# Kernel tuning notes

Measured on AMD Instinct MI355X. Metric: run time of the kernel, lower is better.

## Reference

```python
import jax, jax.numpy as jnp
import numpy as np

GRID_SHAPE = (32, 32)
TEMPERATURE = 1.0


def setup_inputs() -> dict:
    key = jax.random.key(0)
    k1, k2 = jax.random.split(key)
    x = jax.random.normal(k1, (16384, 1024), dtype=jnp.float32)
    som_weights = jax.random.normal(k2, (*GRID_SHAPE, 1024), dtype=jnp.float32) * 0.05
    return {"x": x, "som_weights": som_weights}


def reference(x, som_weights):
    # x: [B, D]; som_weights: [G1, G2, D]
    B, D = x.shape
    g1, g2 = GRID_SHAPE
    w_flat = som_weights.reshape(g1 * g2, D)  # [N, D]
    x_sq = jnp.sum(x * x, axis=-1, keepdims=True)          # [B, 1]
    w_sq = jnp.sum(w_flat * w_flat, axis=-1)[None, :]       # [1, N]
    d2 = x_sq - 2.0 * (x @ w_flat.T) + w_sq                 # [B, N]
    logits = (-d2 / TEMPERATURE).reshape(B, g1, g2)         # [B, G1, G2]
    # per-dimension softmax along each spatial axis, combined multiplicatively
    s1 = jax.nn.softmax(logits, axis=1)
    s2 = jax.nn.softmax(logits, axis=2)
    combined = s1 * s2
    combined = combined / (jnp.sum(combined, axis=(1, 2), keepdims=True) + 1e-8)
    # soft reconstruction: weighted sum over grid of codebook vectors
    recon = jnp.einsum('bn,nd->bd', combined.reshape(B, g1 * g2), w_flat)
    return recon
```

## Files before the change

kernel.cpp:

```cpp
#include <hip/hip_runtime.h>
#include <hip/hip_bf16.h>

static constexpr int BATCH = 16384;
static constexpr int DIM   = 1024;
static constexpr int NN    = 1024;

typedef _Float16 half8  __attribute__((ext_vector_type(8)));
typedef _Float16 half4v __attribute__((ext_vector_type(4)));
typedef float    f32x4  __attribute__((ext_vector_type(4)));

static constexpr float L2E = 1.44269504088896340736f;

__global__ __launch_bounds__(256) void cvt_x_kernel(const float* __restrict__ x,
                                                    _Float16* __restrict__ xh) {
    size_t i = ((size_t)blockIdx.x * 256 + threadIdx.x) * 8;
    f32x4 a = *(const f32x4*)(x + i);
    f32x4 b = *(const f32x4*)(x + i + 4);
    half8 h;
#pragma unroll
    for (int q = 0; q < 4; ++q) { h[q] = (_Float16)a[q]; h[4 + q] = (_Float16)b[q]; }
    *(half8*)(xh + i) = h;
}

__global__ __launch_bounds__(256) void prep_pack_kernel(const float* __restrict__ W,
                                                        _Float16* __restrict__ P1,
                                                        _Float16* __restrict__ P2) {
    const int l = threadIdx.x & 63;
    const int v = threadIdx.x >> 6;
    const int f = blockIdx.x * 4 + v;
    const int hi = f >> 5, lo = f & 31;
    {
        int n  = hi * 16 + (l & 15);
        int k0 = lo * 32 + (l >> 4) * 8;
        const float* src = W + (size_t)n * DIM + k0;
        f32x4 a = *(const f32x4*)src;
        f32x4 b = *(const f32x4*)(src + 4);
        half8 h;
#pragma unroll
        for (int q = 0; q < 4; ++q) { h[q] = (_Float16)a[q]; h[4 + q] = (_Float16)b[q]; }
        *(half8*)(P1 + ((size_t)f * 64 + l) * 8) = h;
    }
    {
        int d  = hi * 16 + (l & 15);
        int n0 = lo * 32 + (l >> 4) * 8;
        half8 h;
#pragma unroll
        for (int j = 0; j < 8; ++j) h[j] = (_Float16)W[(size_t)(n0 + j) * DIM + d];
        *(half8*)(P2 + ((size_t)f * 64 + l) * 8) = h;
    }
}

__global__ __launch_bounds__(256) void wsq_kernel(const float* __restrict__ W,
                                                  float* __restrict__ wsq) {
    const int n = blockIdx.x;
    const int t = threadIdx.x;
    float4 v = *(const float4*)(W + (size_t)n * DIM + 4 * t);
    float ss = v.x * v.x + v.y * v.y + v.z * v.z + v.w * v.w;
#pragma unroll
    for (int o = 32; o > 0; o >>= 1) ss += __shfl_xor(ss, o, 64);
    __shared__ float red[4];
    if ((t & 63) == 0) red[t >> 6] = ss;
    __syncthreads();
    if (t == 0) wsq[n] = red[0] + red[1] + red[2] + red[3];
}

__global__ __launch_bounds__(512, 2) void fused_som_kernel(
    const _Float16* __restrict__ Xh, const _Float16* __restrict__ P1,
    const _Float16* __restrict__ P2, const float* __restrict__ wsq,
    float* __restrict__ Out) {

    __shared__ __align__(16) _Float16 xs[2][64 * 64];
    __shared__ __align__(16) char     BIG[131072];
    __shared__ __align__(16) float    a1_lds[64 * 32];

    const int t  = threadIdx.x;
    const int l  = t & 63;
    const int w  = t >> 6;
    const int r0 = blockIdx.x * 64;

    auto stageA = [&](int buf, int kt) {
        int row = t >> 3;
        int c   = (t & 7) ^ (row & 7);
        const _Float16* g = Xh + (size_t)(r0 + row) * DIM + kt + c * 8;
        __builtin_amdgcn_global_load_lds(
            (const __attribute__((address_space(1))) void*)g,
            (__attribute__((address_space(3))) void*)(&xs[buf][(w * 8) * 64]),
            16, 0, 0);
    };

    f32x4 acc[4][8] = {};
    stageA(0, 0);
    __syncthreads();

    for (int kt = 0; kt < DIM; kt += 64) {
        const int cur = (kt >> 6) & 1;
        const int tk0 = kt >> 5;
        half8 bf0[8], bf1[8];
#pragma unroll
        for (int ni = 0; ni < 8; ++ni) {
            const size_t fb = (size_t)(w * 8 + ni) * 32;
            bf0[ni] = *(const half8*)(P1 + ((fb + tk0) * 64 + l) * 8);
            bf1[ni] = *(const half8*)(P1 + ((fb + tk0 + 1) * 64 + l) * 8);
        }
        if (kt + 64 < DIM) stageA(cur ^ 1, kt + 64);
        half8 af[4];
#pragma unroll
        for (int mi = 0; mi < 4; ++mi) {
            const _Float16* pa = &xs[cur][((l & 15) + mi * 16) * 64];
            af[mi] = *(const half8*)(pa + ((0 + (l >> 4)) ^ (l & 7)) * 8);
        }
#pragma unroll
        for (int mi = 0; mi < 4; ++mi)
#pragma unroll
            for (int ni = 0; ni < 8; ++ni)
                acc[mi][ni] = __builtin_amdgcn_mfma_f32_16x16x32_f16(
                    af[mi], bf0[ni], acc[mi][ni], 0, 0, 0);
#pragma unroll
        for (int mi = 0; mi < 4; ++mi) {
            const _Float16* pa = &xs[cur][((l & 15) + mi * 16) * 64];
            af[mi] = *(const half8*)(pa + ((4 + (l >> 4)) ^ (l & 7)) * 8);
        }
#pragma unroll
        for (int mi = 0; mi < 4; ++mi)
#pragma unroll
            for (int ni = 0; ni < 8; ++ni)
                acc[mi][ni] = __builtin_amdgcn_mfma_f32_16x16x32_f16(
                    af[mi], bf1[ni], acc[mi][ni], 0, 0, 0);
        __syncthreads();
    }

    float wq[8];
#pragma unroll
    for (int ni = 0; ni < 8; ++ni) wq[ni] = wsq[w * 128 + ni * 16 + (l & 15)];
#pragma unroll
    for (int mi = 0; mi < 4; ++mi)
#pragma unroll
        for (int ni = 0; ni < 8; ++ni)
#pragma unroll
            for (int q = 0; q < 4; ++q)
                acc[mi][ni][q] = 2.f * acc[mi][ni][q] - wq[ni];

    float* red = (float*)BIG;

    f32x4 a2v[4][4];
#pragma unroll
    for (int mi = 0; mi < 4; ++mi)
#pragma unroll
        for (int p = 0; p < 4; ++p) {
            f32x4 mx;
#pragma unroll
            for (int q = 0; q < 4; ++q)
                mx[q] = fmaxf(acc[mi][2 * p][q], acc[mi][2 * p + 1][q]);
#pragma unroll
            for (int q = 0; q < 4; ++q) {
                float m = mx[q];
                m = fmaxf(m, __shfl_xor(m, 1, 64));
                m = fmaxf(m, __shfl_xor(m, 2, 64));
                m = fmaxf(m, __shfl_xor(m, 4, 64));
                m = fmaxf(m, __shfl_xor(m, 8, 64));
                mx[q] = m;
            }
#pragma unroll
            for (int q = 0; q < 4; ++q) {
                float s = exp2f((acc[mi][2 * p][q] - mx[q]) * L2E) +
                          exp2f((acc[mi][2 * p + 1][q] - mx[q]) * L2E);
                s += __shfl_xor(s, 1, 64);
                s += __shfl_xor(s, 2, 64);
                s += __shfl_xor(s, 4, 64);
                s += __shfl_xor(s, 8, 64);
                a2v[mi][p][q] = mx[q] * L2E + log2f(s);
            }
        }

#pragma unroll
    for (int mi = 0; mi < 4; ++mi)
#pragma unroll
        for (int j = 0; j < 2; ++j)
#pragma unroll
            for (int q = 0; q < 4; ++q) {
                float pm = fmaxf(fmaxf(acc[mi][j][q], acc[mi][2 + j][q]),
                                 fmaxf(acc[mi][4 + j][q], acc[mi][6 + j][q]));
                int row = mi * 16 + (l >> 4) * 4 + q;
                red[(w * 64 + row) * 33 + j * 16 + (l & 15)] = pm;
            }
    __syncthreads();
#pragma unroll
    for (int i = 0; i < 4; ++i) {
        int pr = t + i * 512;
        int row = pr >> 5, g2 = pr & 31;
        float m = red[row * 33 + g2];
#pragma unroll
        for (int wv = 1; wv < 8; ++wv)
            m = fmaxf(m, red[(wv * 64 + row) * 33 + g2]);
        a1_lds[row * 32 + g2] = m;
    }
    __syncthreads();
#pragma unroll
    for (int mi = 0; mi < 4; ++mi)
#pragma unroll
        for (int j = 0; j < 2; ++j)
#pragma unroll
            for (int q = 0; q < 4; ++q) {
                int row = mi * 16 + (l >> 4) * 4 + q;
                float m1 = a1_lds[row * 32 + j * 16 + (l & 15)];
                float s = 0.f;
#pragma unroll
                for (int p = 0; p < 4; ++p)
                    s += exp2f((acc[mi][2 * p + j][q] - m1) * L2E);
                red[(w * 64 + row) * 33 + j * 16 + (l & 15)] = s;
            }
    __syncthreads();
#pragma unroll
    for (int i = 0; i < 4; ++i) {
        int pr = t + i * 512;
        int row = pr >> 5, g2 = pr & 31;
        float s = 0.f;
#pragma unroll
        for (int wv = 0; wv < 8; ++wv)
            s += red[(wv * 64 + row) * 33 + g2];
        a1_lds[row * 32 + g2] = a1_lds[row * 32 + g2] * L2E + log2f(s);
    }
    __syncthreads();

    float* rowred = (float*)BIG;
#pragma unroll
    for (int mi = 0; mi < 4; ++mi) {
        f32x4 rs = {0.f, 0.f, 0.f, 0.f};
#pragma unroll
        for (int j = 0; j < 2; ++j) {
            f32x4 a1v;
#pragma unroll
            for (int q = 0; q < 4; ++q) {
                int row = mi * 16 + (l >> 4) * 4 + q;
                a1v[q] = a1_lds[row * 32 + j * 16 + (l & 15)];
            }
#pragma unroll
            for (int p = 0; p < 4; ++p)
#pragma unroll
                for (int q = 0; q < 4; ++q) {
                    float cu = exp2f(acc[mi][2 * p + j][q] * (2.f * L2E)
                                     - a1v[q] - a2v[mi][p][q]);
                    acc[mi][2 * p + j][q] = cu;
                    rs[q] += cu;
                }
        }
#pragma unroll
        for (int q = 0; q < 4; ++q) {
            float sv = rs[q];
            sv += __shfl_xor(sv, 1, 64);
            sv += __shfl_xor(sv, 2, 64);
            sv += __shfl_xor(sv, 4, 64);
            sv += __shfl_xor(sv, 8, 64);
            if ((l & 15) == 0) rowred[w * 64 + mi * 16 + (l >> 4) * 4 + q] = sv;
        }
    }
    __syncthreads();
    float* rowinv = ((float*)BIG) + 512;
    if (t < 64) {
        float tot = 0.f;
#pragma unroll
        for (int wv = 0; wv < 8; ++wv) tot += rowred[wv * 64 + t];
        rowinv[t] = 1.f / (tot + 1e-8f);
    }
    __syncthreads();
    f32x4 invr[4];
#pragma unroll
    for (int mi = 0; mi < 4; ++mi)
#pragma unroll
        for (int q = 0; q < 4; ++q)
            invr[mi][q] = rowinv[mi * 16 + (l >> 4) * 4 + q];
    __syncthreads();

    _Float16* cs = (_Float16*)BIG;
#pragma unroll
    for (int mi = 0; mi < 4; ++mi)
#pragma unroll
        for (int ni = 0; ni < 8; ++ni) {
            int chunk = w * 16 + ni * 2 + ((l & 15) >> 3);
#pragma unroll
            for (int q = 0; q < 4; ++q) {
                int row = mi * 16 + (l >> 4) * 4 + q;
                cs[row * 1024 + (chunk ^ (row & 7)) * 8 + (l & 7)] =
                    (_Float16)(acc[mi][ni][q] * invr[mi][q]);
            }
        }
    __syncthreads();

    f32x4 acc2[4][8] = {};
#pragma unroll 2
    for (int kt = 0; kt < NN; kt += 32) {
        const int tn = kt >> 5;
        half8 bf[8], af2[4];
#pragma unroll
        for (int ni = 0; ni < 8; ++ni)
            bf[ni] = *(const half8*)(P2 +
                (((size_t)(w * 8 + ni) * 32 + tn) * 64 + l) * 8);
#pragma unroll
        for (int mi = 0; mi < 4; ++mi) {
            int row = (l & 15) + mi * 16;
            int kc  = tn * 4 + (l >> 4);
            af2[mi] = *(const half8*)(cs + row * 1024 + (kc ^ (row & 7)) * 8);
        }
#pragma unroll
        for (int mi = 0; mi < 4; ++mi)
#pragma unroll
            for (int ni = 0; ni < 8; ++ni)
                acc2[mi][ni] = __builtin_amdgcn_mfma_f32_16x16x32_f16(
                    af2[mi], bf[ni], acc2[mi][ni], 0, 0, 0);
    }

#pragma unroll
    for (int mi = 0; mi < 4; ++mi) {
        const int rbase = r0 + mi * 16 + (l >> 4) * 4;
#pragma unroll
        for (int ni = 0; ni < 8; ++ni) {
            const int col = w * 128 + ni * 16 + (l & 15);
#pragma unroll
            for (int q = 0; q < 4; ++q)
                Out[(size_t)(rbase + q) * DIM + col] = acc2[mi][ni][q];
        }
    }
}

extern "C" void kernel_launch(void* const* d_in, const int* in_sizes, int n_in,
                              void* d_out, int out_size, void* d_ws, size_t ws_size,
                              hipStream_t stream) {
    const float* x = (const float*)d_in[0];
    const float* w = (const float*)d_in[1];
    float* out = (float*)d_out;

    char* ws = (char*)d_ws;
    size_t off = 0;
    _Float16* xh    = (_Float16*)(ws + off); off += (size_t)BATCH * DIM * 2;
    _Float16* pack1 = (_Float16*)(ws + off); off += (size_t)NN * DIM * 2;
    _Float16* pack2 = (_Float16*)(ws + off); off += (size_t)DIM * NN * 2;
    float*    wsq   = (float*)   (ws + off); off += (size_t)NN * 4;

    cvt_x_kernel<<<(BATCH * DIM) / (256 * 8), 256, 0, stream>>>(x, xh);
    prep_pack_kernel<<<512, 256, 0, stream>>>(w, pack1, pack2);
    wsq_kernel<<<NN, 256, 0, stream>>>(w, wsq);
    fused_som_kernel<<<BATCH / 64, 512, 0, stream>>>(xh, pack1, pack2, wsq, out);
}
```

Baseline: 227.4 us.

## Fuse x conversion into main kernel and widen blocks to 1024 threads

Removes the separate fp32-to-fp16 conversion kernel for x. The main kernel now loads fp32 x directly with nontemporal loads, converts it in registers and writes it into the swizzled LDS buffer. It doubles the block size to 16 waves, each covering 64 columns instead of 128, which halves per-thread accumulators. It also writes unnormalized softmax products straight into LDS and applies the row normalization at output time, with nontemporal stores. The aim is to save the extra round trip of the x conversion and one LDS pass, at the risk of more LDS pressure and heavier cross-wave reduction work per block.

```diff
diff --git a/kernel.cpp b/kernel.cpp
--- a/kernel.cpp
+++ b/kernel.cpp
@@ -1,5 +1,4 @@
 #include <hip/hip_runtime.h>
-#include <hip/hip_bf16.h>
 
 static constexpr int BATCH = 16384;
 static constexpr int DIM   = 1024;
@@ -10,17 +9,6 @@
 typedef float    f32x4  __attribute__((ext_vector_type(4)));
 
 static constexpr float L2E = 1.44269504088896340736f;
-
-__global__ __launch_bounds__(256) void cvt_x_kernel(const float* __restrict__ x,
-                                                    _Float16* __restrict__ xh) {
-    size_t i = ((size_t)blockIdx.x * 256 + threadIdx.x) * 8;
-    f32x4 a = *(const f32x4*)(x + i);
-    f32x4 b = *(const f32x4*)(x + i + 4);
-    half8 h;
-#pragma unroll
-    for (int q = 0; q < 4; ++q) { h[q] = (_Float16)a[q]; h[4 + q] = (_Float16)b[q]; }
-    *(half8*)(xh + i) = h;
-}
 
 __global__ __launch_bounds__(256) void prep_pack_kernel(const float* __restrict__ W,
                                                         _Float16* __restrict__ P1,
@@ -64,55 +52,75 @@
     if (t == 0) wsq[n] = red[0] + red[1] + red[2] + red[3];
 }
 
-__global__ __launch_bounds__(512, 2) void fused_som_kernel(
-    const _Float16* __restrict__ Xh, const _Float16* __restrict__ P1,
+__global__ __launch_bounds__(1024, 4) void fused_som_kernel(
+    const float* __restrict__ X, const _Float16* __restrict__ P1,
     const _Float16* __restrict__ P2, const float* __restrict__ wsq,
     float* __restrict__ Out) {
 
     __shared__ __align__(16) _Float16 xs[2][64 * 64];
     __shared__ __align__(16) char     BIG[131072];
     __shared__ __align__(16) float    a1_lds[64 * 32];
+    __shared__ __align__(16) float    rowred[16 * 64];
+    __shared__ __align__(16) float    rowinv[64];
 
     const int t  = threadIdx.x;
     const int l  = t & 63;
     const int w  = t >> 6;
     const int r0 = blockIdx.x * 64;
 
-    auto stageA = [&](int buf, int kt) {
-        int row = t >> 3;
-        int c   = (t & 7) ^ (row & 7);
-        const _Float16* g = Xh + (size_t)(r0 + row) * DIM + kt + c * 8;
-        __builtin_amdgcn_global_load_lds(
-            (const __attribute__((address_space(1))) void*)g,
-            (__attribute__((address_space(3))) void*)(&xs[buf][(w * 8) * 64]),
-            16, 0, 0);
+    auto RIDX = [](int wv, int row, int g2) {
+        return (wv * 64 + row) * 32 + (g2 ^ ((row & 4) << 2));
     };
-
-    f32x4 acc[4][8] = {};
-    stageA(0, 0);
+    auto AIDX = [](int row, int g2) {
+        return row * 32 + (g2 ^ ((row & 4) << 2));
+    };
+
+    const int srow = t >> 4;
+    const int skq  = t & 15;
+
+    auto xload = [&](int kt) -> f32x4 {
+        return __builtin_nontemporal_load(
+            (const f32x4*)(X + (size_t)(r0 + srow) * DIM + kt + skq * 4));
+    };
+    auto xwrite = [&](int buf, f32x4 v) {
+        half4v h;
+        h[0] = (_Float16)v[0]; h[1] = (_Float16)v[1];
+        h[2] = (_Float16)v[2]; h[3] = (_Float16)v[3];
+        int c = skq >> 1;
+        *(half4v*)&xs[buf][srow * 64 + ((c ^ (srow & 7)) << 3) + ((skq & 1) << 2)] = h;
+    };
+
+    f32x4 acc[4][4] = {};
+    {
+        f32x4 xv = xload(0);
+        xwrite(0, xv);
+    }
     __syncthreads();
 
     for (int kt = 0; kt < DIM; kt += 64) {
         const int cur = (kt >> 6) & 1;
+        const bool hasNext = (kt + 64 < DIM);
+        f32x4 xv;
+        if (hasNext) xv = xload(kt + 64);
+
         const int tk0 = kt >> 5;
-        half8 bf0[8], bf1[8];
-#pragma unroll
-        for (int ni = 0; ni < 8; ++ni) {
-            const size_t fb = (size_t)(w * 8 + ni) * 32;
+        half8 bf0[4], bf1[4];
+#pragma unroll
+        for (int ni = 0; ni < 4; ++ni) {
+            const size_t fb = (size_t)(w * 4 + ni) * 32;
             bf0[ni] = *(const half8*)(P1 + ((fb + tk0) * 64 + l) * 8);
             bf1[ni] = *(const half8*)(P1 + ((fb + tk0 + 1) * 64 + l) * 8);
         }
-        if (kt + 64 < DIM) stageA(cur ^ 1, kt + 64);
         half8 af[4];
 #pragma unroll
         for (int mi = 0; mi < 4; ++mi) {
             const _Float16* pa = &xs[cur][((l & 15) + mi * 16) * 64];
-            af[mi] = *(const half8*)(pa + ((0 + (l >> 4)) ^ (l & 7)) * 8);
+            af[mi] = *(const half8*)(pa + (((l >> 4)) ^ (l & 7)) * 8);
         }
 #pragma unroll
         for (int mi = 0; mi < 4; ++mi)
 #pragma unroll
-            for (int ni = 0; ni < 8; ++ni)
+            for (int ni = 0; ni < 4; ++ni)
                 acc[mi][ni] = __builtin_amdgcn_mfma_f32_16x16x32_f16(
                     af[mi], bf0[ni], acc[mi][ni], 0, 0, 0);
 #pragma unroll
@@ -123,30 +131,32 @@
 #pragma unroll
         for (int mi = 0; mi < 4; ++mi)
 #pragma unroll
-            for (int ni = 0; ni < 8; ++ni)
+            for (int ni = 0; ni < 4; ++ni)
                 acc[mi][ni] = __builtin_amdgcn_mfma_f32_16x16x32_f16(
                     af[mi], bf1[ni], acc[mi][ni], 0, 0, 0);
+        __builtin_amdgcn_sched_barrier(0);
+        if (hasNext) xwrite(cur ^ 1, xv);
         __syncthreads();
     }
 
-    float wq[8];
-#pragma unroll
-    for (int ni = 0; ni < 8; ++ni) wq[ni] = wsq[w * 128 + ni * 16 + (l & 15)];
+    float wq[4];
+#pragma unroll
+    for (int ni = 0; ni < 4; ++ni) wq[ni] = wsq[w * 64 + ni * 16 + (l & 15)];
 #pragma unroll
     for (int mi = 0; mi < 4; ++mi)
 #pragma unroll
-        for (int ni = 0; ni < 8; ++ni)
+        for (int ni = 0; ni < 4; ++ni)
 #pragma unroll
             for (int q = 0; q < 4; ++q)
                 acc[mi][ni][q] = 2.f * acc[mi][ni][q] - wq[ni];
 
     float* red = (float*)BIG;
 
-    f32x4 a2v[4][4];
+    f32x4 a2v[4][2];
 #pragma unroll
     for (int mi = 0; mi < 4; ++mi)
 #pragma unroll
-        for (int p = 0; p < 4; ++p) {
+        for (int p = 0; p < 2; ++p) {
             f32x4 mx;
 #pragma unroll
             for (int q = 0; q < 4; ++q)
@@ -178,21 +188,19 @@
         for (int j = 0; j < 2; ++j)
 #pragma unroll
             for (int q = 0; q < 4; ++q) {
-                float pm = fmaxf(fmaxf(acc[mi][j][q], acc[mi][2 + j][q]),
-                                 fmaxf(acc[mi][4 + j][q], acc[mi][6 + j][q]));
                 int row = mi * 16 + (l >> 4) * 4 + q;
-                red[(w * 64 + row) * 33 + j * 16 + (l & 15)] = pm;
-            }
-    __syncthreads();
-#pragma unroll
-    for (int i = 0; i < 4; ++i) {
-        int pr = t + i * 512;
+                red[RIDX(w, row, j * 16 + (l & 15))] =
+                    fmaxf(acc[mi][j][q], acc[mi][2 + j][q]);
+            }
+    __syncthreads();
+#pragma unroll
+    for (int i = 0; i < 2; ++i) {
+        int pr = t + i * 1024;
         int row = pr >> 5, g2 = pr & 31;
-        float m = red[row * 33 + g2];
-#pragma unroll
-        for (int wv = 1; wv < 8; ++wv)
-            m = fmaxf(m, red[(wv * 64 + row) * 33 + g2]);
-        a1_lds[row * 32 + g2] = m;
+        float m = red[RIDX(0, row, g2)];
+#pragma unroll
+        for (int wv = 1; wv < 16; ++wv) m = fmaxf(m, red[RIDX(wv, row, g2)]);
+        a1_lds[AIDX(row, g2)] = m;
     }
     __syncthreads();
 #pragma unroll
@@ -202,27 +210,24 @@
 #pragma unroll
             for (int q = 0; q < 4; ++q) {
                 int row = mi * 16 + (l >> 4) * 4 + q;
-                float m1 = a1_lds[row * 32 + j * 16 + (l & 15)];
-                float s = 0.f;
-#pragma unroll
-                for (int p = 0; p < 4; ++p)
-                    s += exp2f((acc[mi][2 * p + j][q] - m1) * L2E);
-                red[(w * 64 + row) * 33 + j * 16 + (l & 15)] = s;
-            }
-    __syncthreads();
-#pragma unroll
-    for (int i = 0; i < 4; ++i) {
-        int pr = t + i * 512;
+                float m1 = a1_lds[AIDX(row, j * 16 + (l & 15))];
+                float s = exp2f((acc[mi][j][q] - m1) * L2E) +
+                          exp2f((acc[mi][2 + j][q] - m1) * L2E);
+                red[RIDX(w, row, j * 16 + (l & 15))] = s;
+            }
+    __syncthreads();
+#pragma unroll
+    for (int i = 0; i < 2; ++i) {
+        int pr = t + i * 1024;
         int row = pr >> 5, g2 = pr & 31;
         float s = 0.f;
 #pragma unroll
-        for (int wv = 0; wv < 8; ++wv)
-            s += red[(wv * 64 + row) * 33 + g2];
-        a1_lds[row * 32 + g2] = a1_lds[row * 32 + g2] * L2E + log2f(s);
-    }
-    __syncthreads();
-
-    float* rowred = (float*)BIG;
+        for (int wv = 0; wv < 16; ++wv) s += red[RIDX(wv, row, g2)];
+        a1_lds[AIDX(row, g2)] = a1_lds[AIDX(row, g2)] * L2E + log2f(s);
+    }
+    __syncthreads();
+
+    _Float16* cs = (_Float16*)BIG;
 #pragma unroll
     for (int mi = 0; mi < 4; ++mi) {
         f32x4 rs = {0.f, 0.f, 0.f, 0.f};
@@ -232,17 +237,23 @@
 #pragma unroll
             for (int q = 0; q < 4; ++q) {
                 int row = mi * 16 + (l >> 4) * 4 + q;
-                a1v[q] = a1_lds[row * 32 + j * 16 + (l & 15)];
-            }
-#pragma unroll
-            for (int p = 0; p < 4; ++p)
+                a1v[q] = a1_lds[AIDX(row, j * 16 + (l & 15))];
+            }
+#pragma unroll
+            for (int p = 0; p < 2; ++p) {
+                int ni  = 2 * p + j;
+                int col = w * 64 + ni * 16 + (l & 15);
+                int chunk = col >> 3;
 #pragma unroll
                 for (int q = 0; q < 4; ++q) {
-                    float cu = exp2f(acc[mi][2 * p + j][q] * (2.f * L2E)
+                    float cu = exp2f(acc[mi][ni][q] * (2.f * L2E)
                                      - a1v[q] - a2v[mi][p][q]);
-                    acc[mi][2 * p + j][q] = cu;
                     rs[q] += cu;
+                    int row = mi * 16 + (l >> 4) * 4 + q;
+                    cs[row * 1024 + ((chunk ^ (row & 7)) << 3) + (col & 7)] =
+                        (_Float16)cu;
                 }
+            }
         }
 #pragma unroll
         for (int q = 0; q < 4; ++q) {
@@ -255,69 +266,51 @@
         }
     }
     __syncthreads();
-    float* rowinv = ((float*)BIG) + 512;
+
     if (t < 64) {
         float tot = 0.f;
 #pragma unroll
-        for (int wv = 0; wv < 8; ++wv) tot += rowred[wv * 64 + t];
+        for (int wv = 0; wv < 16; ++wv) tot += rowred[wv * 64 + t];
         rowinv[t] = 1.f / (tot + 1e-8f);
     }
-    __syncthreads();
-    f32x4 invr[4];
-#pragma unroll
-    for (int mi = 0; mi < 4; ++mi)
-#pragma unroll
-        for (int q = 0; q < 4; ++q)
-            invr[mi][q] = rowinv[mi * 16 + (l >> 4) * 4 + q];
-    __syncthreads();
-
-    _Float16* cs = (_Float16*)BIG;
-#pragma unroll
-    for (int mi = 0; mi < 4; ++mi)
-#pragma unroll
-        for (int ni = 0; ni < 8; ++ni) {
-            int chunk = w * 16 + ni * 2 + ((l & 15) >> 3);
-#pragma unroll
-            for (int q = 0; q < 4; ++q) {
-                int row = mi * 16 + (l >> 4) * 4 + q;
-                cs[row * 1024 + (chunk ^ (row & 7)) * 8 + (l & 7)] =
-                    (_Float16)(acc[mi][ni][q] * invr[mi][q]);
-            }
-        }
-    __syncthreads();
-
-    f32x4 acc2[4][8] = {};
+
+    f32x4 acc2[4][4] = {};
 #pragma unroll 2
     for (int kt = 0; kt < NN; kt += 32) {
         const int tn = kt >> 5;
-        half8 bf[8], af2[4];
-#pragma unroll
-        for (int ni = 0; ni < 8; ++ni)
+        half8 bf[4], af2[4];
+#pragma unroll
+        for (int ni = 0; ni < 4; ++ni)
             bf[ni] = *(const half8*)(P2 +
-                (((size_t)(w * 8 + ni) * 32 + tn) * 64 + l) * 8);
+                (((size_t)(w * 4 + ni) * 32 + tn) * 64 + l) * 8);
 #pragma unroll
         for (int mi = 0; mi < 4; ++mi) {
             int row = (l & 15) + mi * 16;
             int kc  = tn * 4 + (l >> 4);
-            af2[mi] = *(const half8*)(cs + row * 1024 + (kc ^ (row & 7)) * 8);
+            af2[mi] = *(const half8*)(cs + row * 1024 + ((kc ^ (row & 7)) << 3));
         }
 #pragma unroll
         for (int mi = 0; mi < 4; ++mi)
 #pragma unroll
-            for (int ni = 0; ni < 8; ++ni)
+            for (int ni = 0; ni < 4; ++ni)
                 acc2[mi][ni] = __builtin_amdgcn_mfma_f32_16x16x32_f16(
                     af2[mi], bf[ni], acc2[mi][ni], 0, 0, 0);
     }
+    __syncthreads();
 
 #pragma unroll
     for (int mi = 0; mi < 4; ++mi) {
         const int rbase = r0 + mi * 16 + (l >> 4) * 4;
-#pragma unroll
-        for (int ni = 0; ni < 8; ++ni) {
-            const int col = w * 128 + ni * 16 + (l & 15);
+        f32x4 inv;
+#pragma unroll
+        for (int q = 0; q < 4; ++q) inv[q] = rowinv[mi * 16 + (l >> 4) * 4 + q];
+#pragma unroll
+        for (int ni = 0; ni < 4; ++ni) {
+            const int col = w * 64 + ni * 16 + (l & 15);
 #pragma unroll
             for (int q = 0; q < 4; ++q)
-                Out[(size_t)(rbase + q) * DIM + col] = acc2[mi][ni][q];
+                __builtin_nontemporal_store(acc2[mi][ni][q] * inv[q],
+                    Out + (size_t)(rbase + q) * DIM + col);
         }
     }
 }
@@ -331,13 +324,11 @@
 
     char* ws = (char*)d_ws;
     size_t off = 0;
-    _Float16* xh    = (_Float16*)(ws + off); off += (size_t)BATCH * DIM * 2;
     _Float16* pack1 = (_Float16*)(ws + off); off += (size_t)NN * DIM * 2;
     _Float16* pack2 = (_Float16*)(ws + off); off += (size_t)DIM * NN * 2;
     float*    wsq   = (float*)   (ws + off); off += (size_t)NN * 4;
 
-    cvt_x_kernel<<<(BATCH * DIM) / (256 * 8), 256, 0, stream>>>(x, xh);
     prep_pack_kernel<<<512, 256, 0, stream>>>(w, pack1, pack2);
     wsq_kernel<<<NN, 256, 0, stream>>>(w, wsq);
-    fused_som_kernel<<<BATCH / 64, 512, 0, stream>>>(xh, pack1, pack2, wsq, out);
+    fused_som_kernel<<<BATCH / 64, 1024, 0, stream>>>(x, pack1, pack2, wsq, out);
 }
```

After: 212.8 us. 1.07x faster.
